# Kernel tuning notes

Measured on AMD Instinct MI355X. Metric: run time of the kernel, lower is better.

The kernel has to match this reference:

```python
import jax, jax.numpy as jnp
import numpy as np

N_NODES = 50_000
N_EDGES = 1_600_000
D = 128          # input_dim == hidden_dim
L = 3            # num_layers
NUM_GRAPHS = 64
LN_EPS = 1e-5


def setup_inputs() -> dict:
    key = jax.random.key(0)
    ks = jax.random.split(key, 12)
    x = jax.random.normal(ks[0], (N_NODES, D), dtype=jnp.float32)
    edge_index = jax.random.randint(ks[1], (2, N_EDGES), 0, N_NODES, dtype=jnp.int64)
    edge_weight = jax.random.normal(ks[2], (N_EDGES,), dtype=jnp.float32)  # signed
    batch = jnp.sort(jax.random.randint(ks[3], (N_NODES,), 0, NUM_GRAPHS, dtype=jnp.int64))
    W_pos = jax.random.normal(ks[4], (L, D, D), dtype=jnp.float32) * 0.05
    b_pos = jnp.zeros((L, D), dtype=jnp.float32)
    W_neg = jax.random.normal(ks[5], (L, D, D), dtype=jnp.float32) * 0.05
    b_neg = jnp.zeros((L, D), dtype=jnp.float32)
    ln_gamma = jnp.ones((D,), dtype=jnp.float32)
    ln_beta = jnp.zeros((D,), dtype=jnp.float32)
    return dict(x=x, edge_index=edge_index, edge_weight=edge_weight, batch=batch,
                W_pos=W_pos, b_pos=b_pos, W_neg=W_neg, b_neg=b_neg,
                ln_gamma=ln_gamma, ln_beta=ln_beta)


def gcn_conv(x, src, dst, w, W, b):
    """PyG GCNConv with edge weights: lin -> sym-normalized scatter-add -> +bias.
    Self-loops (weight 1) are handled analytically instead of appending edges.
    Edges with weight 0 contribute nothing (equivalent to sign-masking the edge set)."""
    n = x.shape[0]
    xw = x @ W                                              # [N, D]
    deg = jax.ops.segment_sum(w, dst, num_segments=n) + 1.0  # +1 for self-loop; >= 1
    dinv = jax.lax.rsqrt(deg)                                # deg^{-1/2}
    norm = dinv[src] * w * dinv[dst]                         # [E]
    agg = jax.ops.segment_sum(norm[:, None] * xw[src], dst, num_segments=n)
    agg = agg + (dinv * dinv)[:, None] * xw                  # self-loop message: xw / deg
    return agg + b


def reference(x, edge_index, edge_weight, batch, W_pos, b_pos, W_neg, b_neg, ln_gamma, ln_beta):
    src, dst = edge_index[0], edge_index[1]
    # sign-split as zero-weight edges: identical math to boolean-masked edge subsets
    w_pos = jnp.maximum(edge_weight, 0.0)
    w_neg = jnp.maximum(-edge_weight, 0.0)
    for l in range(L):
        px = gcn_conv(x, src, dst, w_pos, W_pos[l], b_pos[l])
        nx = gcn_conv(x, src, dst, w_neg, W_neg[l], b_neg[l])
        x = jax.nn.relu(px) - jax.nn.relu(nx)
    # global_mean_pool
    sums = jax.ops.segment_sum(x, batch, num_segments=NUM_GRAPHS)
    counts = jax.ops.segment_sum(jnp.ones((x.shape[0],), x.dtype), batch, num_segments=NUM_GRAPHS)
    pooled = sums / jnp.maximum(counts, 1.0)[:, None]        # [G, D]
    # LayerNorm over feature dim
    mu = pooled.mean(-1, keepdims=True)
    var = ((pooled - mu) ** 2).mean(-1, keepdims=True)
    return (pooled - mu) * jax.lax.rsqrt(var + LN_EPS) * ln_gamma + ln_beta
```

## Files before the change

### kernel.cpp

```cpp
#include <hip/hip_runtime.h>
#include <hip/hip_fp16.h>

#define D 128
#define NG 64
#define WPB 4
#define TILE 4096
#define BSH 7
#define BNODES 128
#define CAP 4608
#define MASK40 ((1ULL << 40) - 1)
#define FPSCALE 1048576.0f
#define INV_FPSCALE (1.0f / 1048576.0f)
typedef unsigned int uint;
typedef unsigned long long u64;
typedef _Float16 f16x8 __attribute__((ext_vector_type(8)));
typedef float f32x4 __attribute__((ext_vector_type(4)));

__global__ void k_prep(const float* __restrict__ x, __half* __restrict__ xo,
                       const float* __restrict__ Wp, const float* __restrict__ Wn,
                       __half* __restrict__ wpt, __half* __restrict__ wnt,
                       float* sums, float* cnt, int* bktcur,
                       int total4, int nbuk) {
    int i = blockIdx.x * blockDim.x + threadIdx.x;
    if (i < total4) {
        float4 f = ((const float4*)x)[i];
        __half2 h0 = __floats2half2_rn(f.x, f.y);
        __half2 h1 = __floats2half2_rn(f.z, f.w);
        uint2 st;
        st.x = *(uint*)&h0; st.y = *(uint*)&h1;
        ((uint2*)xo)[i] = st;
    }
    if (i < 3 * 128 * 128) {
        int l = i >> 14;
        int r = i & 16383;
        int col = r >> 7, k = r & 127;
        size_t src = ((size_t)l << 14) + ((size_t)k << 7) + col;
        wpt[i] = __float2half_rn(Wp[src]);
        wnt[i] = __float2half_rn(Wn[src]);
    }
    if (i < NG * D) sums[i] = 0.0f;
    if (i < NG) cnt[i] = 0.0f;
    if (i < nbuk) bktcur[i] = i * CAP;
}

__global__ __launch_bounds__(256) void k_bucket(const int* __restrict__ ei,
                                                const float* __restrict__ ew,
                                                int* bktcur, uint2* rec,
                                                int E, int nbuk) {
    __shared__ int h2[256];
    __shared__ int lofs[512];
    __shared__ int gbase[512];
    __shared__ int lcur[512];
    __shared__ uint2 stg[TILE];
    int t = threadIdx.x;
    lofs[t] = 0; lofs[t + 256] = 0;
    __syncthreads();
    int lo = blockIdx.x * TILE, hi = min(E, lo + TILE);
    int m = hi - lo;
    for (int e = lo + t; e < hi; e += 256)
        atomicAdd(&lofs[ei[(size_t)E + e] >> BSH], 1);
    __syncthreads();
    int c0 = lofs[2 * t], c1 = lofs[2 * t + 1];
    if (c0) gbase[2 * t] = atomicAdd(&bktcur[2 * t], c0);
    if (c1) gbase[2 * t + 1] = atomicAdd(&bktcur[2 * t + 1], c1);
    h2[t] = c0 + c1;
    __syncthreads();
    for (int off = 1; off < 256; off <<= 1) {
        int u = (t >= off) ? h2[t - off] : 0;
        __syncthreads();
        h2[t] += u;
        __syncthreads();
    }
    int excl = h2[t] - (c0 + c1);
    lofs[2 * t] = excl;
    lofs[2 * t + 1] = excl + c0;
    lcur[2 * t] = excl;
    lcur[2 * t + 1] = excl + c0;
    __syncthreads();
    for (int e = lo + t; e < hi; e += 256) {
        int dst = ei[(size_t)E + e];
        int src = ei[e];
        float w = ew[e];
        int b = dst >> BSH;
        int pos = atomicAdd(&lcur[b], 1);
        stg[pos] = make_uint2((uint)src | ((uint)(dst & (BNODES - 1)) << 16) |
                                  ((uint)b << 23),
                              __float_as_uint(w));
    }
    __syncthreads();
    for (int i = t; i < m; i += 256) {
        uint2 r = stg[i];
        int b = (int)(r.x >> 23);
        int gpos = gbase[b] + (i - lofs[b]);
        if (gpos < (b + 1) * CAP)
            rec[gpos] = r;
    }
}

__global__ __launch_bounds__(256) void k_deg(const uint2* __restrict__ rec,
                                             const int* __restrict__ bktcur,
                                             float2* dpn, int* row_ptr,
                                             int* cend, int* cpos, int n) {
    __shared__ u64 accp[BNODES], accn[BNODES];
    __shared__ int s[BNODES];
    int b = blockIdx.x, t = threadIdx.x;
    if (t < BNODES) { accp[t] = 0ULL; accn[t] = 0ULL; }
    __syncthreads();
    int lo = b * CAP, hi = bktcur[b];
    for (int i = lo + t; i < hi; i += 256) {
        uint2 r = rec[i];
        int dl = (r.x >> 16) & (BNODES - 1);
        float w = __uint_as_float(r.y);
        u64 pkt = (1ULL << 40) | (u64)(fabsf(w) * FPSCALE + 0.5f);
        atomicAdd((w < 0.0f) ? &accn[dl] : &accp[dl], pkt);
    }
    __syncthreads();
    int cp = 0, cn = 0, cnt_t = 0;
    u64 p = 0, q = 0;
    if (t < BNODES) {
        p = accp[t]; q = accn[t];
        cp = (int)(p >> 40); cn = (int)(q >> 40);
        cnt_t = cp + cn;
        s[t] = cnt_t;
    }
    __syncthreads();
    for (int off = 1; off < BNODES; off <<= 1) {
        int u = 0;
        if (t < BNODES && t >= off) u = s[t - off];
        __syncthreads();
        if (t < BNODES) s[t] += u;
        __syncthreads();
    }
    if (t < BNODES) {
        int node = b * BNODES + t;
        if (node < n) {
            int base = b * CAP + s[t] - cnt_t;
            row_ptr[node] = base;
            cend[node] = base + cnt_t;
            cpos[node] = cp;
            float2 dd;
            dd.x = rsqrtf(1.0f + (float)(p & MASK40) * INV_FPSCALE);
            dd.y = rsqrtf(1.0f + (float)(q & MASK40) * INV_FPSCALE);
            dpn[node] = dd;
        }
    }
}

__global__ __launch_bounds__(256) void k_csr(const uint2* __restrict__ rec,
                                             const int* __restrict__ bktcur,
                                             const int* __restrict__ row_ptr,
                                             const int* __restrict__ cpos,
                                             const float2* __restrict__ dpn,
                                             uint* pack, int n) {
    __shared__ int curp[BNODES], curn[BNODES];
    int b = blockIdx.x, t = threadIdx.x;
    if (t < BNODES) {
        int node = b * BNODES + t;
        if (node < n) {
            int rp = row_ptr[node];
            curp[t] = rp;
            curn[t] = rp + cpos[node];
        } else { curp[t] = 0; curn[t] = 0; }
    }
    __syncthreads();
    int lo = b * CAP, hi = bktcur[b];
    for (int i = lo + t; i < hi; i += 256) {
        uint2 r = rec[i];
        int src = r.x & 0xFFFFu;
        int dl = (r.x >> 16) & (BNODES - 1);
        float w = __uint_as_float(r.y);
        float2 dd = dpn[src];
        float v;
        int slot;
        if (w < 0.0f) { v = dd.y * (-w); slot = atomicAdd(&curn[dl], 1); }
        else          { v = dd.x * w;    slot = atomicAdd(&curp[dl], 1); }
        pack[slot] = (uint)src | ((uint)__half_as_ushort(__float2half_rn(v)) << 16);
    }
}

__global__ __launch_bounds__(64 * WPB) void k_gather(
    const __half* __restrict__ x16, const uint* __restrict__ pack,
    const int* __restrict__ row_ptr, const int* __restrict__ cend,
    const int* __restrict__ cpos, const float2* __restrict__ dpn,
    __half* __restrict__ tp, __half* __restrict__ tn, int n) {
    __shared__ uint eb[WPB][136];
    const int w = threadIdx.x >> 6;
    const int lane = threadIdx.x & 63;
    const int q = lane >> 4;
    const int c = lane & 15;
    const int node = blockIdx.x * WPB + w;
    if (node >= n) return;
    const int beg = row_ptr[node], end = cend[node];
    const int mid = beg + cpos[node];
    const float2 dd = dpn[node];
    const uint4* __restrict__ x4u = (const uint4*)x16;
    uint* ebw = eb[w];

    uint4 xv = x4u[(size_t)node * 16 + c];
    float xf[8];
    {
        float2 f;
        f = __half22float2(*(__half2*)&xv.x); xf[0] = f.x; xf[1] = f.y;
        f = __half22float2(*(__half2*)&xv.y); xf[2] = f.x; xf[3] = f.y;
        f = __half22float2(*(__half2*)&xv.z); xf[4] = f.x; xf[5] = f.y;
        f = __half22float2(*(__half2*)&xv.w); xf[6] = f.x; xf[7] = f.y;
    }

#pragma unroll
    for (int part = 0; part < 2; ++part) {
        const int lo = part ? mid : beg;
        const int hi = part ? end : mid;
        const float ds = part ? dd.y : dd.x;
        float a0[8], a1[8];
        const float s0 = (q == 0) ? ds : 0.0f;
#pragma unroll
        for (int j = 0; j < 8; ++j) { a0[j] = s0 * xf[j]; a1[j] = 0.0f; }
        for (int cb = lo; cb < hi; cb += 128) {
            int m = hi - cb;
            if (m > 128) m = 128;
            const int mp = (m + 7) & ~7;
            for (int i = lane; i < mp; i += 64)
                ebw[i] = (i < m) ? pack[cb + i] : 0u;
            for (int i = 0; i < mp; i += 8) {
                const uint pk0 = ebw[i + q];
                const uint pk1 = ebw[i + 4 + q];
                const uint4 y0 = x4u[(size_t)(pk0 & 0xFFFFu) * 16 + c];
                const uint4 y1 = x4u[(size_t)(pk1 & 0xFFFFu) * 16 + c];
                const float v0 =
                    __half2float(__ushort_as_half((unsigned short)(pk0 >> 16)));
                const float v1 =
                    __half2float(__ushort_as_half((unsigned short)(pk1 >> 16)));
                float2 f;
                f = __half22float2(*(__half2*)&y0.x);
                a0[0] = fmaf(v0, f.x, a0[0]); a0[1] = fmaf(v0, f.y, a0[1]);
                f = __half22float2(*(__half2*)&y0.y);
                a0[2] = fmaf(v0, f.x, a0[2]); a0[3] = fmaf(v0, f.y, a0[3]);
                f = __half22float2(*(__half2*)&y0.z);
                a0[4] = fmaf(v0, f.x, a0[4]); a0[5] = fmaf(v0, f.y, a0[5]);
                f = __half22float2(*(__half2*)&y0.w);
                a0[6] = fmaf(v0, f.x, a0[6]); a0[7] = fmaf(v0, f.y, a0[7]);
                f = __half22float2(*(__half2*)&y1.x);
                a1[0] = fmaf(v1, f.x, a1[0]); a1[1] = fmaf(v1, f.y, a1[1]);
                f = __half22float2(*(__half2*)&y1.y);
                a1[2] = fmaf(v1, f.x, a1[2]); a1[3] = fmaf(v1, f.y, a1[3]);
                f = __half22float2(*(__half2*)&y1.z);
                a1[4] = fmaf(v1, f.x, a1[4]); a1[5] = fmaf(v1, f.y, a1[5]);
                f = __half22float2(*(__half2*)&y1.w);
                a1[6] = fmaf(v1, f.x, a1[6]); a1[7] = fmaf(v1, f.y, a1[7]);
            }
        }
#pragma unroll
        for (int j = 0; j < 8; ++j) {
            a0[j] += a1[j];
            a0[j] += __shfl_down(a0[j], 32);
            a0[j] += __shfl_down(a0[j], 16);
        }
        if (q == 0) {
            __half2 h0 = __floats2half2_rn(ds * a0[0], ds * a0[1]);
            __half2 h1 = __floats2half2_rn(ds * a0[2], ds * a0[3]);
            __half2 h2 = __floats2half2_rn(ds * a0[4], ds * a0[5]);
            __half2 h3 = __floats2half2_rn(ds * a0[6], ds * a0[7]);
            uint4 st;
            st.x = *(uint*)&h0; st.y = *(uint*)&h1;
            st.z = *(uint*)&h2; st.w = *(uint*)&h3;
            ((uint4*)(part ? tn : tp))[(size_t)node * 16 + c] = st;
        }
    }
}

__global__ __launch_bounds__(256) void k_gemm(
    const __half* __restrict__ tp, const __half* __restrict__ tn,
    const __half* __restrict__ wpt, const __half* __restrict__ wnt,
    const float* __restrict__ bp, const float* __restrict__ bn,
    __half* __restrict__ xout, int nrows) {
    __shared__ __half wlds[2][128][136];
    const int tid = threadIdx.x;
    {
        const uint4* wp4 = (const uint4*)wpt;
        const uint4* wn4 = (const uint4*)wnt;
#pragma unroll
        for (int j = 0; j < 8; ++j) {
            int idx = tid + j * 256;
            int col = idx >> 4;
            int k8 = idx & 15;
            *(uint4*)&wlds[0][col][k8 * 8] = wp4[idx];
            *(uint4*)&wlds[1][col][k8 * 8] = wn4[idx];
        }
    }
    const int wave = tid >> 6;
    const int lane = tid & 63;
    const int cl = lane & 15;
    const int quad = lane >> 4;
    const int row_blk = blockIdx.x * 64 + wave * 16;
    __syncthreads();
    if (row_blk >= nrows) return;
    int arow = row_blk + cl;
    if (arow >= nrows) arow = nrows - 1;
    const f16x8* __restrict__ tpr = (const f16x8*)(tp + (size_t)arow * 128);
    const f16x8* __restrict__ tnr = (const f16x8*)(tn + (size_t)arow * 128);
    f16x8 ap[4], an[4];
#pragma unroll
    for (int kb = 0; kb < 4; ++kb) {
        ap[kb] = tpr[kb * 4 + quad];
        an[kb] = tnr[kb * 4 + quad];
    }
#pragma unroll
    for (int ct = 0; ct < 8; ++ct) {
        const int col = ct * 16 + cl;
        f32x4 accp = {0.0f, 0.0f, 0.0f, 0.0f};
        f32x4 accn = {0.0f, 0.0f, 0.0f, 0.0f};
#pragma unroll
        for (int kb = 0; kb < 4; ++kb) {
            f16x8 wfp = *(const f16x8*)&wlds[0][col][kb * 32 + quad * 8];
            f16x8 wfn = *(const f16x8*)&wlds[1][col][kb * 32 + quad * 8];
            accp = __builtin_amdgcn_mfma_f32_16x16x32_f16(ap[kb], wfp, accp, 0, 0, 0);
            accn = __builtin_amdgcn_mfma_f32_16x16x32_f16(an[kb], wfn, accn, 0, 0, 0);
        }
        const float bpv = bp[col], bnv = bn[col];
#pragma unroll
        for (int reg = 0; reg < 4; ++reg) {
            int row = row_blk + quad * 4 + reg;
            if (row < nrows) {
                float pv = accp[reg] + bpv;
                float nv = accn[reg] + bnv;
                xout[(size_t)row * 128 + col] =
                    __float2half_rn(fmaxf(pv, 0.0f) - fmaxf(nv, 0.0f));
            }
        }
    }
}

__global__ __launch_bounds__(128) void k_pool(
    const __half* __restrict__ x, const int* __restrict__ batch,
    float* sums, float* cnt, int n) {
    int f = threadIdx.x;
    int n0 = blockIdx.x * 64;
    int n1 = min(n0 + 64, n);
    float acc = 0.0f;
    int g_prev = batch[n0];
    int local = 0;
    for (int i = n0; i < n1; ++i) {
        int g = batch[i];
        if (g != g_prev) {
            atomicAdd(&sums[g_prev * D + f], acc);
            if (f == 0) atomicAdd(&cnt[g_prev], (float)local);
            acc = 0.0f; local = 0; g_prev = g;
        }
        acc += __half2float(x[(size_t)i * D + f]);
        local++;
    }
    atomicAdd(&sums[g_prev * D + f], acc);
    if (f == 0) atomicAdd(&cnt[g_prev], (float)local);
}

__global__ __launch_bounds__(128) void k_ln(
    const float* __restrict__ sums, const float* __restrict__ cnt,
    const float* __restrict__ gamma, const float* __restrict__ beta,
    float* __restrict__ out) {
    __shared__ float red[128];
    int g = blockIdx.x, f = threadIdx.x;
    float c = fmaxf(cnt[g], 1.0f);
    float v = sums[g * D + f] / c;
    red[f] = v;
    __syncthreads();
    for (int off = 64; off > 0; off >>= 1) {
        if (f < off) red[f] += red[f + off];
        __syncthreads();
    }
    float mu = red[0] / (float)D;
    __syncthreads();
    float d = v - mu;
    red[f] = d * d;
    __syncthreads();
    for (int off = 64; off > 0; off >>= 1) {
        if (f < off) red[f] += red[f + off];
        __syncthreads();
    }
    float var = red[0] / (float)D;
    out[g * D + f] = d * rsqrtf(var + 1e-5f) * gamma[f] + beta[f];
}

extern "C" void kernel_launch(void* const* d_in, const int* in_sizes, int n_in,
                              void* d_out, int out_size, void* d_ws,
                              size_t ws_size, hipStream_t stream) {
    const float* x     = (const float*)d_in[0];
    const int*   ei    = (const int*)d_in[1];
    const float* ew    = (const float*)d_in[2];
    const int*   bat   = (const int*)d_in[3];
    const float* Wp    = (const float*)d_in[4];
    const float* bp    = (const float*)d_in[5];
    const float* Wn    = (const float*)d_in[6];
    const float* bn    = (const float*)d_in[7];
    const float* gamma = (const float*)d_in[8];
    const float* beta  = (const float*)d_in[9];
    const int n = in_sizes[0] / D;
    const int E = in_sizes[2];
    const int NBUK = (n + BNODES - 1) >> BSH;
    const int NBLK = (E + TILE - 1) / TILE;

    float* ws = (float*)d_ws;
    size_t off = 0;
    auto alloc = [&](size_t elems) {
        float* p = ws + off;
        off += (elems + 63) & ~(size_t)63;
        return p;
    };
    __half* x16  = (__half*)alloc((size_t)n * D / 2);
    __half* tpb  = (__half*)alloc((size_t)n * D / 2);
    __half* tnb  = (__half*)alloc((size_t)n * D / 2);
    __half* xb   = (__half*)alloc((size_t)n * D / 2);
    __half* wpt  = (__half*)alloc(3 * 128 * 128 / 2);
    __half* wnt  = (__half*)alloc(3 * 128 * 128 / 2);
    float2* dpn  = (float2*)alloc((size_t)2 * n);
    float* sums  = alloc(NG * D);
    float* cnt   = alloc(NG);
    int* bktcur  = (int*)alloc(NBUK);
    int* row_ptr = (int*)alloc(n);
    int* cend    = (int*)alloc(n);
    int* cpos    = (int*)alloc(n);
    uint2* rec   = (uint2*)alloc((size_t)NBUK * CAP * 2);
    uint* pack   = (uint*)alloc((size_t)NBUK * CAP);

    k_prep<<<(n * D / 4 + 255) / 256, 256, 0, stream>>>(
        x, x16, Wp, Wn, wpt, wnt, sums, cnt, bktcur, n * D / 4, NBUK);
    k_bucket<<<NBLK, 256, 0, stream>>>(ei, ew, bktcur, rec, E, NBUK);
    k_deg<<<NBUK, 256, 0, stream>>>(rec, bktcur, dpn, row_ptr, cend, cpos, n);
    k_csr<<<NBUK, 256, 0, stream>>>(rec, bktcur, row_ptr, cpos, dpn, pack, n);

    const __half* xcur = x16;
    for (int l = 0; l < 3; ++l) {
        k_gather<<<(n + WPB - 1) / WPB, 64 * WPB, 0, stream>>>(
            xcur, pack, row_ptr, cend, cpos, dpn, tpb, tnb, n);
        k_gemm<<<(n + 63) / 64, 256, 0, stream>>>(
            tpb, tnb, wpt + (size_t)l * 128 * 128, wnt + (size_t)l * 128 * 128,
            bp + (size_t)l * D, bn + (size_t)l * D, xb, n);
        xcur = xb;
    }
    k_pool<<<(n + 63) / 64, 128, 0, stream>>>(xb, bat, sums, cnt, n);
    k_ln<<<NG, 128, 0, stream>>>(sums, cnt, gamma, beta, (float*)d_out);
}
```

Measured before the change: 393.5 us.

## Fuse gather aggregation and MFMA GEMM into a single per-layer kernel

Merges the neighbour-gather kernel and the dense GEMM kernel into one k_layer kernel. Each 256-thread block aggregates 16 nodes into shared memory and then runs the 16-row MFMA transform directly from LDS. Weights are read straight from global or L2 instead of being staged in LDS. This removes the tp/tn intermediate round trip through HBM and one launch per layer. In exchange each wave serially processes 4 nodes, per-block parallelism drops, and the GEMM waits on the slowest node through a block barrier. Layer outputs now ping-pong between two buffers.

Measured after the change: 412.1 us. 1.05x slower.

```diff
diff --git a/kernel.cpp b/kernel.cpp
--- a/kernel.cpp
+++ b/kernel.cpp
@@ -3,7 +3,6 @@
 
 #define D 128
 #define NG 64
-#define WPB 4
 #define TILE 4096
 #define BSH 7
 #define BNODES 128
@@ -178,149 +177,128 @@
     }
 }
 
-__global__ __launch_bounds__(64 * WPB) void k_gather(
-    const __half* __restrict__ x16, const uint* __restrict__ pack,
+__global__ __launch_bounds__(256) void k_layer(
+    const __half* __restrict__ xin, const uint* __restrict__ pack,
     const int* __restrict__ row_ptr, const int* __restrict__ cend,
     const int* __restrict__ cpos, const float2* __restrict__ dpn,
-    __half* __restrict__ tp, __half* __restrict__ tn, int n) {
-    __shared__ uint eb[WPB][136];
+    const __half* __restrict__ wpt, const __half* __restrict__ wnt,
+    const float* __restrict__ bp, const float* __restrict__ bn,
+    __half* __restrict__ xout, int n) {
+    __shared__ uint eb[4][136];
+    __shared__ __half atp[16][136];
+    __shared__ __half atn[16][136];
     const int w = threadIdx.x >> 6;
     const int lane = threadIdx.x & 63;
     const int q = lane >> 4;
     const int c = lane & 15;
-    const int node = blockIdx.x * WPB + w;
-    if (node >= n) return;
-    const int beg = row_ptr[node], end = cend[node];
-    const int mid = beg + cpos[node];
-    const float2 dd = dpn[node];
-    const uint4* __restrict__ x4u = (const uint4*)x16;
+    const int node0 = blockIdx.x * 16;
+    const uint4* __restrict__ x4u = (const uint4*)xin;
     uint* ebw = eb[w];
 
-    uint4 xv = x4u[(size_t)node * 16 + c];
-    float xf[8];
-    {
-        float2 f;
-        f = __half22float2(*(__half2*)&xv.x); xf[0] = f.x; xf[1] = f.y;
-        f = __half22float2(*(__half2*)&xv.y); xf[2] = f.x; xf[3] = f.y;
-        f = __half22float2(*(__half2*)&xv.z); xf[4] = f.x; xf[5] = f.y;
-        f = __half22float2(*(__half2*)&xv.w); xf[6] = f.x; xf[7] = f.y;
-    }
-
-#pragma unroll
-    for (int part = 0; part < 2; ++part) {
-        const int lo = part ? mid : beg;
-        const int hi = part ? end : mid;
-        const float ds = part ? dd.y : dd.x;
-        float a0[8], a1[8];
-        const float s0 = (q == 0) ? ds : 0.0f;
-#pragma unroll
-        for (int j = 0; j < 8; ++j) { a0[j] = s0 * xf[j]; a1[j] = 0.0f; }
-        for (int cb = lo; cb < hi; cb += 128) {
-            int m = hi - cb;
-            if (m > 128) m = 128;
-            const int mp = (m + 7) & ~7;
-            for (int i = lane; i < mp; i += 64)
-                ebw[i] = (i < m) ? pack[cb + i] : 0u;
-            for (int i = 0; i < mp; i += 8) {
-                const uint pk0 = ebw[i + q];
-                const uint pk1 = ebw[i + 4 + q];
-                const uint4 y0 = x4u[(size_t)(pk0 & 0xFFFFu) * 16 + c];
-                const uint4 y1 = x4u[(size_t)(pk1 & 0xFFFFu) * 16 + c];
-                const float v0 =
-                    __half2float(__ushort_as_half((unsigned short)(pk0 >> 16)));
-                const float v1 =
-                    __half2float(__ushort_as_half((unsigned short)(pk1 >> 16)));
-                float2 f;
-                f = __half22float2(*(__half2*)&y0.x);
-                a0[0] = fmaf(v0, f.x, a0[0]); a0[1] = fmaf(v0, f.y, a0[1]);
-                f = __half22float2(*(__half2*)&y0.y);
-                a0[2] = fmaf(v0, f.x, a0[2]); a0[3] = fmaf(v0, f.y, a0[3]);
-                f = __half22float2(*(__half2*)&y0.z);
-                a0[4] = fmaf(v0, f.x, a0[4]); a0[5] = fmaf(v0, f.y, a0[5]);
-                f = __half22float2(*(__half2*)&y0.w);
-                a0[6] = fmaf(v0, f.x, a0[6]); a0[7] = fmaf(v0, f.y, a0[7]);
-                f = __half22float2(*(__half2*)&y1.x);
-                a1[0] = fmaf(v1, f.x, a1[0]); a1[1] = fmaf(v1, f.y, a1[1]);
-                f = __half22float2(*(__half2*)&y1.y);
-                a1[2] = fmaf(v1, f.x, a1[2]); a1[3] = fmaf(v1, f.y, a1[3]);
-                f = __half22float2(*(__half2*)&y1.z);
-                a1[4] = fmaf(v1, f.x, a1[4]); a1[5] = fmaf(v1, f.y, a1[5]);
-                f = __half22float2(*(__half2*)&y1.w);
-                a1[6] = fmaf(v1, f.x, a1[6]); a1[7] = fmaf(v1, f.y, a1[7]);
+    for (int sub = 0; sub < 4; ++sub) {
+        const int node = node0 + w * 4 + sub;
+        if (node >= n) break;
+        const int beg = row_ptr[node], end = cend[node];
+        const int mid = beg + cpos[node];
+        const float2 dd = dpn[node];
+        uint4 xv = x4u[(size_t)node * 16 + c];
+        float xf[8];
+        {
+            float2 f;
+            f = __half22float2(*(__half2*)&xv.x); xf[0] = f.x; xf[1] = f.y;
+            f = __half22float2(*(__half2*)&xv.y); xf[2] = f.x; xf[3] = f.y;
+            f = __half22float2(*(__half2*)&xv.z); xf[4] = f.x; xf[5] = f.y;
+            f = __half22float2(*(__half2*)&xv.w); xf[6] = f.x; xf[7] = f.y;
+        }
+#pragma unroll
+        for (int part = 0; part < 2; ++part) {
+            const int lo = part ? mid : beg;
+            const int hi = part ? end : mid;
+            const float ds = part ? dd.y : dd.x;
+            float a0[8], a1[8];
+            const float s0 = (q == 0) ? ds : 0.0f;
+#pragma unroll
+            for (int j = 0; j < 8; ++j) { a0[j] = s0 * xf[j]; a1[j] = 0.0f; }
+            for (int cb = lo; cb < hi; cb += 128) {
+                int m = hi - cb;
+                if (m > 128) m = 128;
+                const int mp = (m + 7) & ~7;
+                for (int i = lane; i < mp; i += 64)
+                    ebw[i] = (i < m) ? pack[cb + i] : 0u;
+                for (int i = 0; i < mp; i += 8) {
+                    const uint pk0 = ebw[i + q];
+                    const uint pk1 = ebw[i + 4 + q];
+                    const uint4 y0 = x4u[(size_t)(pk0 & 0xFFFFu) * 16 + c];
+                    const uint4 y1 = x4u[(size_t)(pk1 & 0xFFFFu) * 16 + c];
+                    const float v0 = __half2float(
+                        __ushort_as_half((unsigned short)(pk0 >> 16)));
+                    const float v1 = __half2float(
+                        __ushort_as_half((unsigned short)(pk1 >> 16)));
+                    float2 f;
+                    f = __half22float2(*(__half2*)&y0.x);
+                    a0[0] = fmaf(v0, f.x, a0[0]); a0[1] = fmaf(v0, f.y, a0[1]);
+                    f = __half22float2(*(__half2*)&y0.y);
+                    a0[2] = fmaf(v0, f.x, a0[2]); a0[3] = fmaf(v0, f.y, a0[3]);
+                    f = __half22float2(*(__half2*)&y0.z);
+                    a0[4] = fmaf(v0, f.x, a0[4]); a0[5] = fmaf(v0, f.y, a0[5]);
+                    f = __half22float2(*(__half2*)&y0.w);
+                    a0[6] = fmaf(v0, f.x, a0[6]); a0[7] = fmaf(v0, f.y, a0[7]);
+                    f = __half22float2(*(__half2*)&y1.x);
+                    a1[0] = fmaf(v1, f.x, a1[0]); a1[1] = fmaf(v1, f.y, a1[1]);
+                    f = __half22float2(*(__half2*)&y1.y);
+                    a1[2] = fmaf(v1, f.x, a1[2]); a1[3] = fmaf(v1, f.y, a1[3]);
+                    f = __half22float2(*(__half2*)&y1.z);
+                    a1[4] = fmaf(v1, f.x, a1[4]); a1[5] = fmaf(v1, f.y, a1[5]);
+                    f = __half22float2(*(__half2*)&y1.w);
+                    a1[6] = fmaf(v1, f.x, a1[6]); a1[7] = fmaf(v1, f.y, a1[7]);
+                }
             }
-        }
-#pragma unroll
-        for (int j = 0; j < 8; ++j) {
-            a0[j] += a1[j];
-            a0[j] += __shfl_down(a0[j], 32);
-            a0[j] += __shfl_down(a0[j], 16);
-        }
-        if (q == 0) {
-            __half2 h0 = __floats2half2_rn(ds * a0[0], ds * a0[1]);
-            __half2 h1 = __floats2half2_rn(ds * a0[2], ds * a0[3]);
-            __half2 h2 = __floats2half2_rn(ds * a0[4], ds * a0[5]);
-            __half2 h3 = __floats2half2_rn(ds * a0[6], ds * a0[7]);
-            uint4 st;
-            st.x = *(uint*)&h0; st.y = *(uint*)&h1;
-            st.z = *(uint*)&h2; st.w = *(uint*)&h3;
-            ((uint4*)(part ? tn : tp))[(size_t)node * 16 + c] = st;
-        }
-    }
-}
-
-__global__ __launch_bounds__(256) void k_gemm(
-    const __half* __restrict__ tp, const __half* __restrict__ tn,
-    const __half* __restrict__ wpt, const __half* __restrict__ wnt,
-    const float* __restrict__ bp, const float* __restrict__ bn,
-    __half* __restrict__ xout, int nrows) {
-    __shared__ __half wlds[2][128][136];
-    const int tid = threadIdx.x;
-    {
-        const uint4* wp4 = (const uint4*)wpt;
-        const uint4* wn4 = (const uint4*)wnt;
-#pragma unroll
-        for (int j = 0; j < 8; ++j) {
-            int idx = tid + j * 256;
-            int col = idx >> 4;
-            int k8 = idx & 15;
-            *(uint4*)&wlds[0][col][k8 * 8] = wp4[idx];
-            *(uint4*)&wlds[1][col][k8 * 8] = wn4[idx];
-        }
-    }
-    const int wave = tid >> 6;
-    const int lane = tid & 63;
-    const int cl = lane & 15;
-    const int quad = lane >> 4;
-    const int row_blk = blockIdx.x * 64 + wave * 16;
-    __syncthreads();
-    if (row_blk >= nrows) return;
-    int arow = row_blk + cl;
-    if (arow >= nrows) arow = nrows - 1;
-    const f16x8* __restrict__ tpr = (const f16x8*)(tp + (size_t)arow * 128);
-    const f16x8* __restrict__ tnr = (const f16x8*)(tn + (size_t)arow * 128);
-    f16x8 ap[4], an[4];
+#pragma unroll
+            for (int j = 0; j < 8; ++j) {
+                a0[j] += a1[j];
+                a0[j] += __shfl_down(a0[j], 32);
+                a0[j] += __shfl_down(a0[j], 16);
+            }
+            if (q == 0) {
+                __half2 h0 = __floats2half2_rn(ds * a0[0], ds * a0[1]);
+                __half2 h1 = __floats2half2_rn(ds * a0[2], ds * a0[3]);
+                __half2 h2 = __floats2half2_rn(ds * a0[4], ds * a0[5]);
+                __half2 h3 = __floats2half2_rn(ds * a0[6], ds * a0[7]);
+                uint4 st;
+                st.x = *(uint*)&h0; st.y = *(uint*)&h1;
+                st.z = *(uint*)&h2; st.w = *(uint*)&h3;
+                __half* dstrow = part ? atn[w * 4 + sub] : atp[w * 4 + sub];
+                *(uint4*)&dstrow[c * 8] = st;
+            }
+        }
+    }
+    __syncthreads();
+
+    f16x8 apf[4], anf[4];
 #pragma unroll
     for (int kb = 0; kb < 4; ++kb) {
-        ap[kb] = tpr[kb * 4 + quad];
-        an[kb] = tnr[kb * 4 + quad];
-    }
-#pragma unroll
-    for (int ct = 0; ct < 8; ++ct) {
-        const int col = ct * 16 + cl;
+        apf[kb] = *(const f16x8*)&atp[c][kb * 32 + q * 8];
+        anf[kb] = *(const f16x8*)&atn[c][kb * 32 + q * 8];
+    }
+#pragma unroll
+    for (int t2 = 0; t2 < 2; ++t2) {
+        const int col = (w * 2 + t2) * 16 + c;
+        const f16x8* __restrict__ wpr = (const f16x8*)(wpt + (size_t)col * 128);
+        const f16x8* __restrict__ wnr = (const f16x8*)(wnt + (size_t)col * 128);
         f32x4 accp = {0.0f, 0.0f, 0.0f, 0.0f};
         f32x4 accn = {0.0f, 0.0f, 0.0f, 0.0f};
 #pragma unroll
         for (int kb = 0; kb < 4; ++kb) {
-            f16x8 wfp = *(const f16x8*)&wlds[0][col][kb * 32 + quad * 8];
-            f16x8 wfn = *(const f16x8*)&wlds[1][col][kb * 32 + quad * 8];
-            accp = __builtin_amdgcn_mfma_f32_16x16x32_f16(ap[kb], wfp, accp, 0, 0, 0);
-            accn = __builtin_amdgcn_mfma_f32_16x16x32_f16(an[kb], wfn, accn, 0, 0, 0);
+            accp = __builtin_amdgcn_mfma_f32_16x16x32_f16(apf[kb], wpr[kb * 4 + q],
+                                                          accp, 0, 0, 0);
+            accn = __builtin_amdgcn_mfma_f32_16x16x32_f16(anf[kb], wnr[kb * 4 + q],
+                                                          accn, 0, 0, 0);
         }
         const float bpv = bp[col], bnv = bn[col];
 #pragma unroll
         for (int reg = 0; reg < 4; ++reg) {
-            int row = row_blk + quad * 4 + reg;
-            if (row < nrows) {
+            int row = node0 + q * 4 + reg;
+            if (row < n) {
                 float pv = accp[reg] + bpv;
                 float nv = accn[reg] + bnv;
                 xout[(size_t)row * 128 + col] =
@@ -406,9 +384,8 @@
         return p;
     };
     __half* x16  = (__half*)alloc((size_t)n * D / 2);
-    __half* tpb  = (__half*)alloc((size_t)n * D / 2);
-    __half* tnb  = (__half*)alloc((size_t)n * D / 2);
-    __half* xb   = (__half*)alloc((size_t)n * D / 2);
+    __half* xba  = (__half*)alloc((size_t)n * D / 2);
+    __half* xbb  = (__half*)alloc((size_t)n * D / 2);
     __half* wpt  = (__half*)alloc(3 * 128 * 128 / 2);
     __half* wnt  = (__half*)alloc(3 * 128 * 128 / 2);
     float2* dpn  = (float2*)alloc((size_t)2 * n);
@@ -427,15 +404,14 @@
     k_deg<<<NBUK, 256, 0, stream>>>(rec, bktcur, dpn, row_ptr, cend, cpos, n);
     k_csr<<<NBUK, 256, 0, stream>>>(rec, bktcur, row_ptr, cpos, dpn, pack, n);
 
-    const __half* xcur = x16;
+    const __half* lin[3]  = {x16, xba, xbb};
+    __half*       lout[3] = {xba, xbb, xba};
     for (int l = 0; l < 3; ++l) {
-        k_gather<<<(n + WPB - 1) / WPB, 64 * WPB, 0, stream>>>(
-            xcur, pack, row_ptr, cend, cpos, dpn, tpb, tnb, n);
-        k_gemm<<<(n + 63) / 64, 256, 0, stream>>>(
-            tpb, tnb, wpt + (size_t)l * 128 * 128, wnt + (size_t)l * 128 * 128,
-            bp + (size_t)l * D, bn + (size_t)l * D, xb, n);
-        xcur = xb;
-    }
-    k_pool<<<(n + 63) / 64, 128, 0, stream>>>(xb, bat, sums, cnt, n);
+        k_layer<<<(n + 15) / 16, 256, 0, stream>>>(
+            lin[l], pack, row_ptr, cend, cpos, dpn,
+            wpt + (size_t)l * 128 * 128, wnt + (size_t)l * 128 * 128,
+            bp + (size_t)l * D, bn + (size_t)l * D, lout[l], n);
+    }
+    k_pool<<<(n + 63) / 64, 128, 0, stream>>>(xba, bat, sums, cnt, n);
     k_ln<<<NG, 128, 0, stream>>>(sums, cnt, gamma, beta, (float*)d_out);
 }
```
